# Kernel tuning notes

Hardware: AMD Instinct MI355X
Metric: run time of the kernel (lower is better)

## Reference

```python
import jax, jax.numpy as jnp
import numpy as np

NUM_STAGES = 3
EPS = 1e-6


def _l2norm(x, axis):
    return x / (EPS + jnp.linalg.norm(x, axis=axis, keepdims=True))


def _l1norm(x, axis):
    return x / (EPS + jnp.sum(x, axis=axis, keepdims=True))


def setup_inputs() -> dict:
    key = jax.random.key(0)
    k1, k2 = jax.random.split(key)
    B, C, H, W, K = 16, 512, 64, 64, 64
    feats = jax.random.normal(k1, (B, C, H, W), dtype=jnp.float32)
    # bases buffer: N(0, sqrt(2/K)) then l2-normalized along channel dim (done in reference)
    bases = jax.random.normal(k2, (1, C, K), dtype=jnp.float32) * np.sqrt(2.0 / K)
    return {"feats": feats, "bases": bases}


def reference(feats, bases):
    B, C, H, W = feats.shape
    f = feats.reshape(B, C, H * W)              # [B, C, N]
    b = _l2norm(bases, axis=1)                  # match buffer init normalization
    b = jnp.broadcast_to(b, (B, C, b.shape[2])) # [B, C, K]
    attention = None
    for _ in range(NUM_STAGES):
        attention = jnp.einsum('bcn,bck->bnk', f, b)        # [B, N, K]
        attention = jax.nn.softmax(attention, axis=2)
        attention_normed = _l1norm(attention, axis=1)
        b = jnp.einsum('bcn,bnk->bck', f, attention_normed)  # [B, C, K]
        b = _l2norm(b, axis=1)
    # EM loop runs under torch.no_grad in the original
    b = jax.lax.stop_gradient(b)
    attention = jax.lax.stop_gradient(attention)
    feats_recon = jnp.einsum('bck,bnk->bcn', b, attention)   # [B, C, N]
    return feats_recon.reshape(B, C, H, W)
```

## Files before the change

kernel.cpp:

```cpp
#include <hip/hip_runtime.h>
#include <stdint.h>

#define B_ 16
#define C_ 512
#define N_ 4096
#define K_ 64
#define NUM_STAGES 3

typedef __bf16 bf16x8 __attribute__((ext_vector_type(8)));
typedef float f32x4 __attribute__((ext_vector_type(4)));

__device__ __forceinline__ uint16_t f2bf(float x) {
  union { float f; uint32_t u; } v; v.f = x;
  uint32_t r = (v.u + 0x7FFFu + ((v.u >> 16) & 1u)) >> 16;
  return (uint16_t)r;
}

__device__ __forceinline__ void async16(const uint16_t* g, uint16_t* l) {
  __builtin_amdgcn_global_load_lds(
      (const __attribute__((address_space(1))) unsigned int*)g,
      (__attribute__((address_space(3))) unsigned int*)l, 16, 0, 0);
}

__global__ __launch_bounds__(256) void k_prep(const float* __restrict__ feats,
                                              uint16_t* __restrict__ f16,
                                              uint16_t* __restrict__ fT16) {
  __shared__ uint16_t tile[64][65];
  int b = blockIdx.z, c0 = blockIdx.y * 64, n0 = blockIdx.x * 64;
  int t = threadIdx.x;
  const float* src = feats + ((size_t)b * C_ + c0) * N_ + n0;
  uint16_t* dst = f16 + ((size_t)b * C_ + c0) * N_ + n0;
  int cl = t >> 4;
  int nl = (t & 15) * 4;
#pragma unroll
  for (int i = 0; i < 4; ++i) {
    int c = cl + 16 * i;
    float4 v = *(const float4*)(src + (size_t)c * N_ + nl);
    ushort4 x;
    x.x = f2bf(v.x); x.y = f2bf(v.y); x.z = f2bf(v.z); x.w = f2bf(v.w);
    *(ushort4*)(dst + (size_t)c * N_ + nl) = x;
    tile[c][nl + 0] = x.x; tile[c][nl + 1] = x.y;
    tile[c][nl + 2] = x.z; tile[c][nl + 3] = x.w;
  }
  __syncthreads();
  uint16_t* dstT = fT16 + ((size_t)b * N_ + n0) * C_ + c0;
#pragma unroll
  for (int i = 0; i < 4; ++i) {
    int n = cl + 16 * i;
    int c = nl;
    ushort4 y;
    y.x = tile[c + 0][n]; y.y = tile[c + 1][n];
    y.z = tile[c + 2][n]; y.w = tile[c + 3][n];
    *(ushort4*)(dstT + (size_t)n * C_ + c) = y;
  }
}

__global__ __launch_bounds__(256) void k_init_basis(const float* __restrict__ bases,
                                                    uint16_t* __restrict__ basis,
                                                    uint16_t* __restrict__ basisT) {
  int b = blockIdx.x;
  int t = threadIdx.x;
  __shared__ float red[256];
  __shared__ float inv[64];
  int k = t & 63;
  float s = 0.f;
  for (int c = (t >> 6); c < C_; c += 4) {
    float v = bases[c * K_ + k];
    s += v * v;
  }
  red[t] = s;
  __syncthreads();
  if (t < 64) {
    float tot = red[t] + red[t + 64] + red[t + 128] + red[t + 192];
    inv[t] = 1.f / (1e-6f + sqrtf(tot));
  }
  __syncthreads();
  uint16_t* ob = basis + (size_t)b * C_ * K_;
  for (int i = 0; i < (C_ * K_) / 256; ++i) {
    int idx = t + 256 * i;
    int kk = idx & 63;
    ob[idx] = f2bf(bases[idx] * inv[kk]);
  }
  uint16_t* obT = basisT + (size_t)b * K_ * C_;
  for (int i = 0; i < (C_ * K_) / 256; ++i) {
    int idx = t + 256 * i;
    int kk = idx >> 9;
    int cc = idx & 511;
    obT[idx] = f2bf(bases[cc * K_ + kk] * inv[kk]);
  }
}

__global__ __launch_bounds__(256) void k_gemm1(const uint16_t* __restrict__ fT,
                                               const uint16_t* __restrict__ basisT,
                                               uint16_t* __restrict__ attn,
                                               uint16_t* __restrict__ attnT,
                                               int write_attn) {
  __shared__ __attribute__((aligned(16))) uint16_t ldsA[64 * 64];
  __shared__ __attribute__((aligned(16))) uint16_t ldsB[64 * 64];
  int b = blockIdx.y;
  int n0 = blockIdx.x * 64;
  int t = threadIdx.x;
  int w = t >> 6, lane = t & 63, l15 = lane & 15, quad = lane >> 4;
  const uint16_t* A = fT + ((size_t)b * N_ + n0) * C_;
  const uint16_t* Bm = basisT + (size_t)b * K_ * C_;
  f32x4 acc[4] = {};
  for (int cs = 0; cs < C_; cs += 64) {
    __syncthreads();
#pragma unroll
    for (int r = 0; r < 2; ++r) {
      int e = r * 256 + t;
      int row = e >> 3, ch = e & 7;
      int sch = (ch + row) & 7;
      async16(A + (size_t)row * C_ + cs + sch * 8, ldsA + (r * 256 + (t & 192)) * 8);
    }
#pragma unroll
    for (int r = 0; r < 2; ++r) {
      int e = r * 256 + t;
      int row = e >> 3, ch = e & 7;
      int sch = (ch + row) & 7;
      async16(Bm + (size_t)row * C_ + cs + sch * 8, ldsB + (r * 256 + (t & 192)) * 8);
    }
    __syncthreads();
#pragma unroll
    for (int s = 0; s < 2; ++s) {
      int cc = s * 4 + quad;
      int ra = 16 * w + l15;
      bf16x8 af = *(const bf16x8*)(ldsA + (ra * 8 + ((cc - ra) & 7)) * 8);
#pragma unroll
      for (int t4 = 0; t4 < 4; ++t4) {
        int rb = 16 * t4 + l15;
        bf16x8 bv = *(const bf16x8*)(ldsB + (rb * 8 + ((cc - rb) & 7)) * 8);
        acc[t4] = __builtin_amdgcn_mfma_f32_16x16x32_bf16(af, bv, acc[t4], 0, 0, 0);
      }
    }
  }
  float p[4][4];
#pragma unroll
  for (int r = 0; r < 4; ++r) {
    float m = fmaxf(fmaxf(acc[0][r], acc[1][r]), fmaxf(acc[2][r], acc[3][r]));
    m = fmaxf(m, __shfl_xor(m, 1));
    m = fmaxf(m, __shfl_xor(m, 2));
    m = fmaxf(m, __shfl_xor(m, 4));
    m = fmaxf(m, __shfl_xor(m, 8));
    float s = 0.f;
#pragma unroll
    for (int t4 = 0; t4 < 4; ++t4) { p[t4][r] = __expf(acc[t4][r] - m); s += p[t4][r]; }
    s += __shfl_xor(s, 1); s += __shfl_xor(s, 2);
    s += __shfl_xor(s, 4); s += __shfl_xor(s, 8);
    float inv = 1.f / s;
#pragma unroll
    for (int t4 = 0; t4 < 4; ++t4) p[t4][r] *= inv;
  }
  if (write_attn) {
    uint16_t* oa = attn + ((size_t)b * N_ + n0 + 16 * w + quad * 4) * K_;
#pragma unroll
    for (int r = 0; r < 4; ++r) {
#pragma unroll
      for (int t4 = 0; t4 < 4; ++t4) oa[(size_t)r * K_ + 16 * t4 + l15] = f2bf(p[t4][r]);
    }
  }
#pragma unroll
  for (int t4 = 0; t4 < 4; ++t4) {
    ushort4 y;
    y.x = f2bf(p[t4][0]); y.y = f2bf(p[t4][1]);
    y.z = f2bf(p[t4][2]); y.w = f2bf(p[t4][3]);
    *(ushort4*)(attnT + ((size_t)b * K_ + 16 * t4 + l15) * N_ + n0 + 16 * w + quad * 4) = y;
  }
}

__global__ __launch_bounds__(256) void k_gemm2(const uint16_t* __restrict__ f16,
                                               const uint16_t* __restrict__ attnT,
                                               float* __restrict__ brawT) {
  __shared__ __attribute__((aligned(16))) uint16_t ldsA[32 * 64];
  __shared__ __attribute__((aligned(16))) uint16_t ldsB[64 * 64];
  int b = blockIdx.z;
  int c0 = blockIdx.x * 32;
  int slice = blockIdx.y;
  int ns0 = slice * 1024;
  int t = threadIdx.x, w = t >> 6, lane = t & 63, l15 = lane & 15, quad = lane >> 4;
  int h = w >> 1, kh = w & 1;
  const uint16_t* A = f16 + ((size_t)b * C_ + c0) * N_;
  const uint16_t* Bm = attnT + (size_t)b * K_ * N_;
  f32x4 acc[2] = {};
  for (int ns = ns0; ns < ns0 + 1024; ns += 64) {
    __syncthreads();
    {
      int row = t >> 3, ch = t & 7;
      int sch = (ch + row) & 7;
      async16(A + (size_t)row * N_ + ns + sch * 8, ldsA + (t & 192) * 8);
    }
#pragma unroll
    for (int r = 0; r < 2; ++r) {
      int e = r * 256 + t;
      int row = e >> 3, ch = e & 7;
      int sch = (ch + row) & 7;
      async16(Bm + (size_t)row * N_ + ns + sch * 8, ldsB + (r * 256 + (t & 192)) * 8);
    }
    __syncthreads();
#pragma unroll
    for (int s = 0; s < 2; ++s) {
      int cc = s * 4 + quad;
      int ra = 16 * h + l15;
      bf16x8 af = *(const bf16x8*)(ldsA + (ra * 8 + ((cc - ra) & 7)) * 8);
#pragma unroll
      for (int t2 = 0; t2 < 2; ++t2) {
        int rb = 32 * kh + 16 * t2 + l15;
        bf16x8 bv = *(const bf16x8*)(ldsB + (rb * 8 + ((cc - rb) & 7)) * 8);
        acc[t2] = __builtin_amdgcn_mfma_f32_16x16x32_bf16(af, bv, acc[t2], 0, 0, 0);
      }
    }
  }
  float* out = brawT + ((size_t)slice * B_ + b) * K_ * C_;
#pragma unroll
  for (int t2 = 0; t2 < 2; ++t2) {
    int k = 32 * kh + 16 * t2 + l15;
    float4 v = make_float4(acc[t2][0], acc[t2][1], acc[t2][2], acc[t2][3]);
    *(float4*)(out + (size_t)k * C_ + c0 + 16 * h + quad * 4) = v;
  }
}

__global__ __launch_bounds__(256) void k_l2fused(const float* __restrict__ brawT,
                                                 uint16_t* __restrict__ basisT,
                                                 uint16_t* __restrict__ basis) {
  __shared__ float red[4][128];
  __shared__ float invs[4];
  int b = blockIdx.x, kg = blockIdx.y;
  int t = threadIdx.x;
  int c4 = (t & 127) * 4;
  int khalf = t >> 7;
  float4 bs[2];
  float pr[2];
#pragma unroll
  for (int i = 0; i < 2; ++i) {
    int k = kg * 4 + khalf * 2 + i;
    float4 a = make_float4(0.f, 0.f, 0.f, 0.f);
#pragma unroll
    for (int s = 0; s < 4; ++s) {
      const float* rp = brawT + (((size_t)s * B_ + b) * K_ + k) * C_ + c4;
      float4 v = *(const float4*)rp;
      a.x += v.x; a.y += v.y; a.z += v.z; a.w += v.w;
    }
    bs[i] = a;
    pr[i] = a.x * a.x + a.y * a.y + a.z * a.z + a.w * a.w;
  }
  red[khalf * 2 + 0][t & 127] = pr[0];
  red[khalf * 2 + 1][t & 127] = pr[1];
  __syncthreads();
  if (t < 4) {
    float s = 0.f;
#pragma unroll
    for (int j = 0; j < 128; ++j) s += red[t][j];
    invs[t] = 1.f / (1e-6f + sqrtf(s));
  }
  __syncthreads();
#pragma unroll
  for (int i = 0; i < 2; ++i) {
    int kk = khalf * 2 + i;
    int k = kg * 4 + kk;
    float inv = invs[kk];
    ushort4 y;
    y.x = f2bf(bs[i].x * inv); y.y = f2bf(bs[i].y * inv);
    y.z = f2bf(bs[i].z * inv); y.w = f2bf(bs[i].w * inv);
    *(ushort4*)(basisT + ((size_t)b * K_ + k) * C_ + c4) = y;
    uint16_t* ob = basis + (size_t)b * C_ * K_ + k;
    ob[(size_t)(c4 + 0) * K_] = y.x;
    ob[(size_t)(c4 + 1) * K_] = y.y;
    ob[(size_t)(c4 + 2) * K_] = y.z;
    ob[(size_t)(c4 + 3) * K_] = y.w;
  }
}

__global__ __launch_bounds__(256) void k_recon(const uint16_t* __restrict__ attn,
                                               const uint16_t* __restrict__ basis,
                                               float* __restrict__ out) {
  __shared__ __attribute__((aligned(16))) char smem[64 * 68 * 4];
  uint16_t* ldsA = (uint16_t*)smem;
  uint16_t* ldsB = (uint16_t*)(smem + 8192);
  float* ldsT = (float*)smem;
  int b = blockIdx.z, c0 = blockIdx.y * 64, n0 = blockIdx.x * 64;
  int t = threadIdx.x, w = t >> 6, lane = t & 63, l15 = lane & 15, quad = lane >> 4;
  const uint16_t* A = attn + ((size_t)b * N_ + n0) * K_;
  const uint16_t* Bm = basis + ((size_t)b * C_ + c0) * K_;
#pragma unroll
  for (int r = 0; r < 2; ++r) {
    int e = r * 256 + t;
    int row = e >> 3, ch = e & 7, sch = (ch + row) & 7;
    async16(A + (size_t)row * K_ + sch * 8, ldsA + (r * 256 + (t & 192)) * 8);
  }
#pragma unroll
  for (int r = 0; r < 2; ++r) {
    int e = r * 256 + t;
    int row = e >> 3, ch = e & 7, sch = (ch + row) & 7;
    async16(Bm + (size_t)row * K_ + sch * 8, ldsB + (r * 256 + (t & 192)) * 8);
  }
  f32x4 acc[4] = {};
  __syncthreads();
#pragma unroll
  for (int s = 0; s < 2; ++s) {
    int cc = s * 4 + quad;
    int ra = 16 * w + l15;
    bf16x8 af = *(const bf16x8*)(ldsA + (ra * 8 + ((cc - ra) & 7)) * 8);
#pragma unroll
    for (int t4 = 0; t4 < 4; ++t4) {
      int rb = 16 * t4 + l15;
      bf16x8 bv = *(const bf16x8*)(ldsB + (rb * 8 + ((cc - rb) & 7)) * 8);
      acc[t4] = __builtin_amdgcn_mfma_f32_16x16x32_bf16(af, bv, acc[t4], 0, 0, 0);
    }
  }
  __syncthreads();
#pragma unroll
  for (int t4 = 0; t4 < 4; ++t4) {
    float4 v = make_float4(acc[t4][0], acc[t4][1], acc[t4][2], acc[t4][3]);
    *(float4*)(ldsT + (size_t)(16 * t4 + l15) * 68 + 16 * w + quad * 4) = v;
  }
  __syncthreads();
  float* op = out + ((size_t)b * C_ + c0) * N_ + n0;
#pragma unroll
  for (int j = 0; j < 16; ++j) {
    int c = 4 * j + w;
    op[(size_t)c * N_ + lane] = ldsT[(size_t)c * 68 + lane];
  }
}

extern "C" void kernel_launch(void* const* d_in, const int* in_sizes, int n_in,
                              void* d_out, int out_size, void* d_ws, size_t ws_size,
                              hipStream_t stream) {
  const float* feats = (const float*)d_in[0];
  const float* bases = (const float*)d_in[1];
  float* out = (float*)d_out;
  char* ws = (char*)d_ws;
  uint16_t* f16 = (uint16_t*)(ws);
  uint16_t* fT16 = (uint16_t*)(ws + 67108864);
  uint16_t* attn = (uint16_t*)(ws + 134217728);
  uint16_t* attnT = (uint16_t*)(ws + 142606336);
  uint16_t* basis = (uint16_t*)(ws + 150994944);
  uint16_t* basisT = (uint16_t*)(ws + 152043520);
  float* brawT = (float*)(ws + 153092096);

  k_prep<<<dim3(64, 8, 16), 256, 0, stream>>>(feats, f16, fT16);
  k_init_basis<<<16, 256, 0, stream>>>(bases, basis, basisT);
  for (int st = 0; st < NUM_STAGES; ++st) {
    k_gemm1<<<dim3(64, 16), 256, 0, stream>>>(fT16, basisT, attn, attnT,
                                              st == NUM_STAGES - 1 ? 1 : 0);
    k_gemm2<<<dim3(16, 4, 16), 256, 0, stream>>>(f16, attnT, brawT);
    k_l2fused<<<dim3(16, 16), 256, 0, stream>>>(brawT, basisT, basis);
  }
  k_recon<<<dim3(64, 8, 16), 256, 0, stream>>>(attn, basis, out);
}
```

Baseline: 447.6 us.

## Double-buffer LDS staging in GEMM kernels and software-pipeline the prep transpose

The two GEMM kernels now use double-buffered LDS tiles: the next K-chunk is issued with async global-to-LDS loads before computing on the current one, with explicit vmcnt waits and barriers. The prep kernel handles four 64-column tiles per block, prefetching the next tile's floats into registers while converting and transposing the current one through a double-buffered LDS tile. The goal is to hide global-memory latency behind MFMA and conversion work. In exchange, LDS use doubles, the prep grid has fewer blocks, and correctness relies on hand-set waitcnt values.

```diff
diff --git a/kernel.cpp b/kernel.cpp
--- a/kernel.cpp
+++ b/kernel.cpp
@@ -22,36 +22,70 @@
       (__attribute__((address_space(3))) unsigned int*)l, 16, 0, 0);
 }
 
+__device__ __forceinline__ void stage64x64(const uint16_t* g, size_t ld, int cs,
+                                           uint16_t* lds, int t) {
+#pragma unroll
+  for (int r = 0; r < 2; ++r) {
+    int e = r * 256 + t;
+    int row = e >> 3, ch = e & 7;
+    int sch = (ch + row) & 7;
+    async16(g + (size_t)row * ld + cs + sch * 8, lds + (r * 256 + (t & 192)) * 8);
+  }
+}
+
+__device__ __forceinline__ void stage32x64(const uint16_t* g, size_t ld, int cs,
+                                           uint16_t* lds, int t) {
+  int row = t >> 3, ch = t & 7;
+  int sch = (ch + row) & 7;
+  async16(g + (size_t)row * ld + cs + sch * 8, lds + (t & 192) * 8);
+}
+
 __global__ __launch_bounds__(256) void k_prep(const float* __restrict__ feats,
                                               uint16_t* __restrict__ f16,
                                               uint16_t* __restrict__ fT16) {
-  __shared__ uint16_t tile[64][65];
-  int b = blockIdx.z, c0 = blockIdx.y * 64, n0 = blockIdx.x * 64;
+  __shared__ uint16_t tile[2][64][65];
+  int b = blockIdx.z, c0 = blockIdx.y * 64, n0 = blockIdx.x * 256;
   int t = threadIdx.x;
+  int cl = t >> 4;
+  int nl = (t & 15) * 4;
   const float* src = feats + ((size_t)b * C_ + c0) * N_ + n0;
   uint16_t* dst = f16 + ((size_t)b * C_ + c0) * N_ + n0;
-  int cl = t >> 4;
-  int nl = (t & 15) * 4;
-#pragma unroll
-  for (int i = 0; i < 4; ++i) {
-    int c = cl + 16 * i;
-    float4 v = *(const float4*)(src + (size_t)c * N_ + nl);
-    ushort4 x;
-    x.x = f2bf(v.x); x.y = f2bf(v.y); x.z = f2bf(v.z); x.w = f2bf(v.w);
-    *(ushort4*)(dst + (size_t)c * N_ + nl) = x;
-    tile[c][nl + 0] = x.x; tile[c][nl + 1] = x.y;
-    tile[c][nl + 2] = x.z; tile[c][nl + 3] = x.w;
-  }
-  __syncthreads();
   uint16_t* dstT = fT16 + ((size_t)b * N_ + n0) * C_ + c0;
-#pragma unroll
-  for (int i = 0; i < 4; ++i) {
-    int n = cl + 16 * i;
-    int c = nl;
-    ushort4 y;
-    y.x = tile[c + 0][n]; y.y = tile[c + 1][n];
-    y.z = tile[c + 2][n]; y.w = tile[c + 3][n];
-    *(ushort4*)(dstT + (size_t)n * C_ + c) = y;
+  float4 rr[2][4];
+#pragma unroll
+  for (int i = 0; i < 4; ++i)
+    rr[0][i] = *(const float4*)(src + (size_t)(cl + 16 * i) * N_ + nl);
+#pragma unroll
+  for (int s = 0; s < 4; ++s) {
+    const int cur = s & 1;
+    if (s < 3) {
+#pragma unroll
+      for (int i = 0; i < 4; ++i)
+        rr[cur ^ 1][i] =
+            *(const float4*)(src + (size_t)(cl + 16 * i) * N_ + (s + 1) * 64 + nl);
+    }
+#pragma unroll
+    for (int i = 0; i < 4; ++i) {
+      int c = cl + 16 * i;
+      float4 v = rr[cur][i];
+      ushort4 x;
+      x.x = f2bf(v.x); x.y = f2bf(v.y); x.z = f2bf(v.z); x.w = f2bf(v.w);
+      *(ushort4*)(dst + (size_t)c * N_ + s * 64 + nl) = x;
+      tile[cur][c][nl + 0] = x.x; tile[cur][c][nl + 1] = x.y;
+      tile[cur][c][nl + 2] = x.z; tile[cur][c][nl + 3] = x.w;
+    }
+    asm volatile("s_waitcnt lgkmcnt(0)" ::: "memory");
+    __builtin_amdgcn_s_barrier();
+    __builtin_amdgcn_sched_barrier(0);
+#pragma unroll
+    for (int i = 0; i < 4; ++i) {
+      int n = cl + 16 * i;
+      int c = nl;
+      ushort4 y;
+      y.x = tile[cur][c + 0][n]; y.y = tile[cur][c + 1][n];
+      y.z = tile[cur][c + 2][n]; y.w = tile[cur][c + 3][n];
+      *(ushort4*)(dstT + (size_t)(s * 64 + n) * C_ + c) = y;
+    }
   }
 }
 
@@ -95,8 +129,8 @@
                                                uint16_t* __restrict__ attn,
                                                uint16_t* __restrict__ attnT,
                                                int write_attn) {
-  __shared__ __attribute__((aligned(16))) uint16_t ldsA[64 * 64];
-  __shared__ __attribute__((aligned(16))) uint16_t ldsB[64 * 64];
+  __shared__ __attribute__((aligned(16))) uint16_t ldsA[2][64 * 64];
+  __shared__ __attribute__((aligned(16))) uint16_t ldsB[2][64 * 64];
   int b = blockIdx.y;
   int n0 = blockIdx.x * 64;
   int t = threadIdx.x;
@@ -104,35 +138,37 @@
   const uint16_t* A = fT + ((size_t)b * N_ + n0) * C_;
   const uint16_t* Bm = basisT + (size_t)b * K_ * C_;
   f32x4 acc[4] = {};
-  for (int cs = 0; cs < C_; cs += 64) {
-    __syncthreads();
-#pragma unroll
-    for (int r = 0; r < 2; ++r) {
-      int e = r * 256 + t;
-      int row = e >> 3, ch = e & 7;
-      int sch = (ch + row) & 7;
-      async16(A + (size_t)row * C_ + cs + sch * 8, ldsA + (r * 256 + (t & 192)) * 8);
-    }
-#pragma unroll
-    for (int r = 0; r < 2; ++r) {
-      int e = r * 256 + t;
-      int row = e >> 3, ch = e & 7;
-      int sch = (ch + row) & 7;
-      async16(Bm + (size_t)row * C_ + cs + sch * 8, ldsB + (r * 256 + (t & 192)) * 8);
-    }
-    __syncthreads();
+  stage64x64(A, C_, 0, ldsA[0], t);
+  stage64x64(Bm, C_, 0, ldsB[0], t);
+#pragma unroll
+  for (int it = 0; it < 8; ++it) {
+    const int cur = it & 1;
+    if (it < 7) {
+      stage64x64(A, C_, (it + 1) * 64, ldsA[cur ^ 1], t);
+      stage64x64(Bm, C_, (it + 1) * 64, ldsB[cur ^ 1], t);
+      __builtin_amdgcn_sched_barrier(0);
+      asm volatile("s_waitcnt vmcnt(4)" ::: "memory");
+    } else {
+      asm volatile("s_waitcnt vmcnt(0)" ::: "memory");
+    }
+    __builtin_amdgcn_s_barrier();
+    __builtin_amdgcn_sched_barrier(0);
+    const uint16_t* lA = ldsA[cur];
+    const uint16_t* lB = ldsB[cur];
 #pragma unroll
     for (int s = 0; s < 2; ++s) {
       int cc = s * 4 + quad;
       int ra = 16 * w + l15;
-      bf16x8 af = *(const bf16x8*)(ldsA + (ra * 8 + ((cc - ra) & 7)) * 8);
+      bf16x8 af = *(const bf16x8*)(lA + (ra * 8 + ((cc - ra) & 7)) * 8);
 #pragma unroll
       for (int t4 = 0; t4 < 4; ++t4) {
         int rb = 16 * t4 + l15;
-        bf16x8 bv = *(const bf16x8*)(ldsB + (rb * 8 + ((cc - rb) & 7)) * 8);
+        bf16x8 bv = *(const bf16x8*)(lB + (rb * 8 + ((cc - rb) & 7)) * 8);
         acc[t4] = __builtin_amdgcn_mfma_f32_16x16x32_bf16(af, bv, acc[t4], 0, 0, 0);
       }
     }
+    __builtin_amdgcn_sched_barrier(0);
+    __builtin_amdgcn_s_barrier();
   }
   float p[4][4];
 #pragma unroll
@@ -171,8 +207,8 @@
 __global__ __launch_bounds__(256) void k_gemm2(const uint16_t* __restrict__ f16,
                                                const uint16_t* __restrict__ attnT,
                                                float* __restrict__ brawT) {
-  __shared__ __attribute__((aligned(16))) uint16_t ldsA[32 * 64];
-  __shared__ __attribute__((aligned(16))) uint16_t ldsB[64 * 64];
+  __shared__ __attribute__((aligned(16))) uint16_t ldsA[2][32 * 64];
+  __shared__ __attribute__((aligned(16))) uint16_t ldsB[2][64 * 64];
   int b = blockIdx.z;
   int c0 = blockIdx.x * 32;
   int slice = blockIdx.y;
@@ -182,33 +218,38 @@
   const uint16_t* A = f16 + ((size_t)b * C_ + c0) * N_;
   const uint16_t* Bm = attnT + (size_t)b * K_ * N_;
   f32x4 acc[2] = {};
-  for (int ns = ns0; ns < ns0 + 1024; ns += 64) {
-    __syncthreads();
-    {
-      int row = t >> 3, ch = t & 7;
-      int sch = (ch + row) & 7;
-      async16(A + (size_t)row * N_ + ns + sch * 8, ldsA + (t & 192) * 8);
-    }
-#pragma unroll
-    for (int r = 0; r < 2; ++r) {
-      int e = r * 256 + t;
-      int row = e >> 3, ch = e & 7;
-      int sch = (ch + row) & 7;
-      async16(Bm + (size_t)row * N_ + ns + sch * 8, ldsB + (r * 256 + (t & 192)) * 8);
-    }
-    __syncthreads();
+  stage32x64(A, N_, ns0, ldsA[0], t);
+  stage64x64(Bm, N_, ns0, ldsB[0], t);
+#pragma unroll
+  for (int it = 0; it < 16; ++it) {
+    const int cur = it & 1;
+    if (it < 15) {
+      int ns = ns0 + (it + 1) * 64;
+      stage32x64(A, N_, ns, ldsA[cur ^ 1], t);
+      stage64x64(Bm, N_, ns, ldsB[cur ^ 1], t);
+      __builtin_amdgcn_sched_barrier(0);
+      asm volatile("s_waitcnt vmcnt(3)" ::: "memory");
+    } else {
+      asm volatile("s_waitcnt vmcnt(0)" ::: "memory");
+    }
+    __builtin_amdgcn_s_barrier();
+    __builtin_amdgcn_sched_barrier(0);
+    const uint16_t* lA = ldsA[cur];
+    const uint16_t* lB = ldsB[cur];
 #pragma unroll
     for (int s = 0; s < 2; ++s) {
       int cc = s * 4 + quad;
       int ra = 16 * h + l15;
-      bf16x8 af = *(const bf16x8*)(ldsA + (ra * 8 + ((cc - ra) & 7)) * 8);
+      bf16x8 af = *(const bf16x8*)(lA + (ra * 8 + ((cc - ra) & 7)) * 8);
 #pragma unroll
       for (int t2 = 0; t2 < 2; ++t2) {
         int rb = 32 * kh + 16 * t2 + l15;
-        bf16x8 bv = *(const bf16x8*)(ldsB + (rb * 8 + ((cc - rb) & 7)) * 8);
+        bf16x8 bv = *(const bf16x8*)(lB + (rb * 8 + ((cc - rb) & 7)) * 8);
         acc[t2] = __builtin_amdgcn_mfma_f32_16x16x32_bf16(af, bv, acc[t2], 0, 0, 0);
       }
     }
+    __builtin_amdgcn_sched_barrier(0);
+    __builtin_amdgcn_s_barrier();
   }
   float* out = brawT + ((size_t)slice * B_ + b) * K_ * C_;
 #pragma unroll
@@ -337,7 +378,7 @@
   uint16_t* basisT = (uint16_t*)(ws + 152043520);
   float* brawT = (float*)(ws + 153092096);
 
-  k_prep<<<dim3(64, 8, 16), 256, 0, stream>>>(feats, f16, fT16);
+  k_prep<<<dim3(16, 8, 16), 256, 0, stream>>>(feats, f16, fT16);
   k_init_basis<<<16, 256, 0, stream>>>(bases, basis, basisT);
   for (int st = 0; st < NUM_STAGES; ++st) {
     k_gemm1<<<dim3(64, 16), 256, 0, stream>>>(fT16, basisT, attn, attnT,
```

New measurement: 455.9 us. No clear change (+1.8%).

## Load MFMA operands directly from global memory, stage whole basis in LDS

Applied to the files above, without the earlier changes.

k_gemm1 now runs 512-thread blocks over 128 rows. It preloads the entire 64x512 basis for the batch into LDS once with an XOR swizzle, and the A fragments come straight from global memory, so the per-chunk barrier loop is gone. k_gemm2 and k_recon drop LDS staging altogether and read both MFMA operands directly from global memory, relying on cache reuse. This removes sync and LDS round-trips, but it risks uncoalesced 16-byte strided global loads and higher LDS use per block in gemm1 (64KB).

```diff
diff --git a/kernel.cpp b/kernel.cpp
--- a/kernel.cpp
+++ b/kernel.cpp
@@ -90,46 +90,38 @@
   }
 }
 
-__global__ __launch_bounds__(256) void k_gemm1(const uint16_t* __restrict__ fT,
-                                               const uint16_t* __restrict__ basisT,
-                                               uint16_t* __restrict__ attn,
-                                               uint16_t* __restrict__ attnT,
-                                               int write_attn) {
-  __shared__ __attribute__((aligned(16))) uint16_t ldsA[64 * 64];
-  __shared__ __attribute__((aligned(16))) uint16_t ldsB[64 * 64];
+__global__ __launch_bounds__(512, 4) void k_gemm1(const uint16_t* __restrict__ fT,
+                                                  const uint16_t* __restrict__ basisT,
+                                                  uint16_t* __restrict__ attn,
+                                                  uint16_t* __restrict__ attnT,
+                                                  int write_attn) {
+  __shared__ __attribute__((aligned(16))) uint16_t ldsB[K_ * C_];
   int b = blockIdx.y;
-  int n0 = blockIdx.x * 64;
+  int n0 = blockIdx.x * 128;
   int t = threadIdx.x;
   int w = t >> 6, lane = t & 63, l15 = lane & 15, quad = lane >> 4;
-  const uint16_t* A = fT + ((size_t)b * N_ + n0) * C_;
   const uint16_t* Bm = basisT + (size_t)b * K_ * C_;
+#pragma unroll
+  for (int r = 0; r < 8; ++r) {
+    int o = r * 512 + t;
+    int rb = o >> 6;
+    int v = o & 63;
+    int m = v ^ (rb & 7);
+    async16(Bm + (size_t)rb * C_ + m * 8, ldsB + (r * 512 + (t & 448)) * 8);
+  }
+  const uint16_t* A = fT + ((size_t)b * N_ + n0 + 16 * w + l15) * C_;
   f32x4 acc[4] = {};
-  for (int cs = 0; cs < C_; cs += 64) {
-    __syncthreads();
-#pragma unroll
-    for (int r = 0; r < 2; ++r) {
-      int e = r * 256 + t;
-      int row = e >> 3, ch = e & 7;
-      int sch = (ch + row) & 7;
-      async16(A + (size_t)row * C_ + cs + sch * 8, ldsA + (r * 256 + (t & 192)) * 8);
-    }
-#pragma unroll
-    for (int r = 0; r < 2; ++r) {
-      int e = r * 256 + t;
-      int row = e >> 3, ch = e & 7;
-      int sch = (ch + row) & 7;
-      async16(Bm + (size_t)row * C_ + cs + sch * 8, ldsB + (r * 256 + (t & 192)) * 8);
-    }
-    __syncthreads();
+  __syncthreads();
+#pragma unroll
+  for (int it = 0; it < 8; ++it) {
 #pragma unroll
     for (int s = 0; s < 2; ++s) {
-      int cc = s * 4 + quad;
-      int ra = 16 * w + l15;
-      bf16x8 af = *(const bf16x8*)(ldsA + (ra * 8 + ((cc - ra) & 7)) * 8);
+      int m = it * 8 + s * 4 + quad;
+      bf16x8 af = *(const bf16x8*)(A + m * 8);
 #pragma unroll
       for (int t4 = 0; t4 < 4; ++t4) {
         int rb = 16 * t4 + l15;
-        bf16x8 bv = *(const bf16x8*)(ldsB + (rb * 8 + ((cc - rb) & 7)) * 8);
+        bf16x8 bv = *(const bf16x8*)(ldsB + ((size_t)rb * 64 + (m ^ (rb & 7))) * 8);
         acc[t4] = __builtin_amdgcn_mfma_f32_16x16x32_bf16(af, bv, acc[t4], 0, 0, 0);
       }
     }
@@ -168,44 +160,27 @@
   }
 }
 
-__global__ __launch_bounds__(256) void k_gemm2(const uint16_t* __restrict__ f16,
-                                               const uint16_t* __restrict__ attnT,
-                                               float* __restrict__ brawT) {
-  __shared__ __attribute__((aligned(16))) uint16_t ldsA[32 * 64];
-  __shared__ __attribute__((aligned(16))) uint16_t ldsB[64 * 64];
+__global__ __launch_bounds__(256, 4) void k_gemm2(const uint16_t* __restrict__ f16,
+                                                  const uint16_t* __restrict__ attnT,
+                                                  float* __restrict__ brawT) {
   int b = blockIdx.z;
   int c0 = blockIdx.x * 32;
   int slice = blockIdx.y;
   int ns0 = slice * 1024;
   int t = threadIdx.x, w = t >> 6, lane = t & 63, l15 = lane & 15, quad = lane >> 4;
   int h = w >> 1, kh = w & 1;
-  const uint16_t* A = f16 + ((size_t)b * C_ + c0) * N_;
-  const uint16_t* Bm = attnT + (size_t)b * K_ * N_;
+  const uint16_t* A = f16 + ((size_t)b * C_ + c0 + 16 * h + l15) * N_;
+  const uint16_t* Bm = attnT + ((size_t)b * K_ + 32 * kh) * N_;
   f32x4 acc[2] = {};
-  for (int ns = ns0; ns < ns0 + 1024; ns += 64) {
-    __syncthreads();
-    {
-      int row = t >> 3, ch = t & 7;
-      int sch = (ch + row) & 7;
-      async16(A + (size_t)row * N_ + ns + sch * 8, ldsA + (t & 192) * 8);
-    }
-#pragma unroll
-    for (int r = 0; r < 2; ++r) {
-      int e = r * 256 + t;
-      int row = e >> 3, ch = e & 7;
-      int sch = (ch + row) & 7;
-      async16(Bm + (size_t)row * N_ + ns + sch * 8, ldsB + (r * 256 + (t & 192)) * 8);
-    }
-    __syncthreads();
+#pragma unroll 4
+  for (int it = 0; it < 16; ++it) {
 #pragma unroll
     for (int s = 0; s < 2; ++s) {
-      int cc = s * 4 + quad;
-      int ra = 16 * h + l15;
-      bf16x8 af = *(const bf16x8*)(ldsA + (ra * 8 + ((cc - ra) & 7)) * 8);
+      int n = ns0 + it * 64 + (s * 4 + quad) * 8;
+      bf16x8 af = *(const bf16x8*)(A + n);
 #pragma unroll
       for (int t2 = 0; t2 < 2; ++t2) {
-        int rb = 32 * kh + 16 * t2 + l15;
-        bf16x8 bv = *(const bf16x8*)(ldsB + (rb * 8 + ((cc - rb) & 7)) * 8);
+        bf16x8 bv = *(const bf16x8*)(Bm + (size_t)(16 * t2 + l15) * N_ + n);
         acc[t2] = __builtin_amdgcn_mfma_f32_16x16x32_bf16(af, bv, acc[t2], 0, 0, 0);
       }
     }
@@ -273,41 +248,22 @@
 __global__ __launch_bounds__(256) void k_recon(const uint16_t* __restrict__ attn,
                                                const uint16_t* __restrict__ basis,
                                                float* __restrict__ out) {
-  __shared__ __attribute__((aligned(16))) char smem[64 * 68 * 4];
-  uint16_t* ldsA = (uint16_t*)smem;
-  uint16_t* ldsB = (uint16_t*)(smem + 8192);
-  float* ldsT = (float*)smem;
+  __shared__ __attribute__((aligned(16))) float ldsT[64 * 68];
   int b = blockIdx.z, c0 = blockIdx.y * 64, n0 = blockIdx.x * 64;
   int t = threadIdx.x, w = t >> 6, lane = t & 63, l15 = lane & 15, quad = lane >> 4;
-  const uint16_t* A = attn + ((size_t)b * N_ + n0) * K_;
+  const uint16_t* A = attn + ((size_t)b * N_ + n0 + 16 * w + l15) * K_;
   const uint16_t* Bm = basis + ((size_t)b * C_ + c0) * K_;
-#pragma unroll
-  for (int r = 0; r < 2; ++r) {
-    int e = r * 256 + t;
-    int row = e >> 3, ch = e & 7, sch = (ch + row) & 7;
-    async16(A + (size_t)row * K_ + sch * 8, ldsA + (r * 256 + (t & 192)) * 8);
-  }
-#pragma unroll
-  for (int r = 0; r < 2; ++r) {
-    int e = r * 256 + t;
-    int row = e >> 3, ch = e & 7, sch = (ch + row) & 7;
-    async16(Bm + (size_t)row * K_ + sch * 8, ldsB + (r * 256 + (t & 192)) * 8);
-  }
   f32x4 acc[4] = {};
-  __syncthreads();
 #pragma unroll
   for (int s = 0; s < 2; ++s) {
-    int cc = s * 4 + quad;
-    int ra = 16 * w + l15;
-    bf16x8 af = *(const bf16x8*)(ldsA + (ra * 8 + ((cc - ra) & 7)) * 8);
+    int cc = (s * 4 + quad) * 8;
+    bf16x8 af = *(const bf16x8*)(A + cc);
 #pragma unroll
     for (int t4 = 0; t4 < 4; ++t4) {
-      int rb = 16 * t4 + l15;
-      bf16x8 bv = *(const bf16x8*)(ldsB + (rb * 8 + ((cc - rb) & 7)) * 8);
+      bf16x8 bv = *(const bf16x8*)(Bm + (size_t)(16 * t4 + l15) * K_ + cc);
       acc[t4] = __builtin_amdgcn_mfma_f32_16x16x32_bf16(af, bv, acc[t4], 0, 0, 0);
     }
   }
-  __syncthreads();
 #pragma unroll
   for (int t4 = 0; t4 < 4; ++t4) {
     float4 v = make_float4(acc[t4][0], acc[t4][1], acc[t4][2], acc[t4][3]);
@@ -340,7 +296,7 @@
   k_prep<<<dim3(64, 8, 16), 256, 0, stream>>>(feats, f16, fT16);
   k_init_basis<<<16, 256, 0, stream>>>(bases, basis, basisT);
   for (int st = 0; st < NUM_STAGES; ++st) {
-    k_gemm1<<<dim3(64, 16), 256, 0, stream>>>(fT16, basisT, attn, attnT,
+    k_gemm1<<<dim3(32, 16), 512, 0, stream>>>(fT16, basisT, attn, attnT,
                                               st == NUM_STAGES - 1 ? 1 : 0);
     k_gemm2<<<dim3(16, 4, 16), 256, 0, stream>>>(f16, attnT, brawT);
     k_l2fused<<<dim3(16, 16), 256, 0, stream>>>(brawT, basisT, basis);
```

Result: slower. 538.0 us (+20.2%).
